# Optimization experiments

Hardware: AMD Instinct MI355X
Metric: run time of the kernel (lower is better)

## Reference

```python
import jax, jax.numpy as jnp
import numpy as np
from jax import lax

# Hardcoded geometry from the module (npatch=4, padding16=1, padding32=2)
GLO_MUL, GLO_RES = 16, 18   # 64/4, 64/4 + 2*1
LOC_MUL, LOC_RES = 32, 36   # 128/4, 128/4 + 2*2
C_FEAT = 16                 # PointNetfeatLocal output channels


def point_to_cell(pts, feat, R):
    """Scatter per-point features into a dense R^3 grid (last write wins,
    matching torch advanced-indexing assignment). pts: (B,N,3) float coords
    already clamped to [0, R-1]; feat: (B,N,C). Returns (B,C,R,R,R)."""
    B, N, C = feat.shape
    idx = pts.astype(jnp.int32)
    bidx = jnp.broadcast_to(jnp.arange(B)[:, None], (B, N))
    grid = jnp.zeros((B, R, R, R, C), feat.dtype)
    grid = grid.at[bidx, idx[..., 0], idx[..., 1], idx[..., 2]].set(feat)
    return jnp.transpose(grid, (0, 4, 1, 2, 3))


def setup_inputs() -> dict:
    key = jax.random.key(0)
    ks = jax.random.split(key, 8)
    B = 4
    # points live in [-0.5, 0.5) so that x*128 + 64.5 lands inside the grid
    curves = jax.random.uniform(ks[0], (B, 8192, 3), jnp.float32) - 0.5
    surfaces = jax.random.uniform(ks[1], (B, 24576, 3), jnp.float32) - 0.5
    occupany64_softmax = jax.random.uniform(ks[2], (B, 2, 64, 64, 64), jnp.float32)
    indices_array = jax.random.randint(ks[3], (B, 16), 0, 64, jnp.int32)
    W1 = jax.random.normal(ks[4], (128, 3), jnp.float32) * 0.1
    b1 = jnp.zeros((128,), jnp.float32)
    W2 = jax.random.normal(ks[5], (16, 128), jnp.float32) * 0.1
    b2 = jnp.zeros((16,), jnp.float32)
    return dict(curves=curves, surfaces=surfaces,
                occupany64_softmax=occupany64_softmax,
                indices_array=indices_array, W1=W1, b1=b1, W2=W2, b2=b2)


def reference(curves, surfaces, occupany64_softmax, indices_array, W1, b1, W2, b2):
    # --- PointNetfeatLocal: two 1x1 Conv1d == per-point MLP 3->128->16 ---
    x = jnp.concatenate([curves, surfaces], axis=1)            # (B, N, 3)
    h = jax.nn.relu(jnp.einsum('bnd,cd->bnc', x, W1) + b1)      # (B, N, 128)
    feat_pt = jnp.einsum('bnc,oc->bno', h, W2) + b2             # (B, N, 16)

    # --- pad occupancy (padding16=1) ---
    occ_pad = jnp.pad(occupany64_softmax,
                      ((0, 0), (0, 0), (1, 1), (1, 1), (1, 1)))  # (B,2,66,66,66)

    # --- batch_grid_pooling128 + padding32=2 ---
    cube128 = jnp.clip(x * 128.0 + 64.5, 0.0, 127.0)
    cell128 = point_to_cell(cube128, feat_pt, 128)              # (B,16,128,128,128)
    cell128_pad = jnp.pad(cell128,
                          ((0, 0), (0, 0), (2, 2), (2, 2), (2, 2)))  # (B,16,132^3)

    # --- crop_global_local_patches (vectorized via vmap'd dynamic_slice) ---
    B, P = indices_array.shape
    bb = jnp.repeat(jnp.arange(B), P)
    pp = indices_array.reshape(-1).astype(jnp.int32)

    def crop_one(b, p):
        i, j, k = p // 16, (p % 16) // 4, p % 4
        g = lax.dynamic_slice(occ_pad,
                              (b, 0, i * GLO_MUL, j * GLO_MUL, k * GLO_MUL),
                              (1, 2, GLO_RES, GLO_RES, GLO_RES))[0]
        l = lax.dynamic_slice(cell128_pad,
                              (b, 0, i * LOC_MUL, j * LOC_MUL, k * LOC_MUL),
                              (1, C_FEAT, LOC_RES, LOC_RES, LOC_RES))[0]
        return g, l

    global_patches, local_patches = jax.vmap(crop_one)(bb, pp)
    # global_patches: (B*P, 2, 18, 18, 18); local_patches: (B*P, 16, 36, 36, 36)
    return global_patches, local_patches
```

## Files before the change

kernel.cpp:

```cpp
#include <hip/hip_runtime.h>

#define BATCH   4
#define NCUR    8192
#define NSUR    24576
#define NPTS    (NCUR + NSUR)
#define NPATCH  64
#define GS      18
#define LS      36
#define GVOL    (GS*GS*GS)
#define LVOL    (LS*LS*LS)
#define GOUT_TOTAL (NPATCH*2*GVOL)
#define GBLOCKS (GOUT_TOTAL/256)
#define MBLOCKS ((BATCH*NPTS)/256)
#define LBLOCKS ((NPATCH*LVOL + 255)/256)

template<int CTRL>
__device__ __forceinline__ float qperm(float x) {
    return __builtin_bit_cast(float, __builtin_amdgcn_mov_dpp(
        __builtin_bit_cast(int, x), CTRL, 0xF, 0xF, true));
}
#define QP_B0 0x00
#define QP_B1 0x55
#define QP_B2 0xAA
#define QP_B3 0xFF
#define QP_X1 0xB1
#define QP_X2 0x4E

__global__ __launch_bounds__(256)
void mlp_scatter_global_kernel(const float* __restrict__ curves,
                               const float* __restrict__ surfaces,
                               const float* __restrict__ W1,
                               const float* __restrict__ b1,
                               const float* __restrict__ W2,
                               const float* __restrict__ b2,
                               const float* __restrict__ occ,
                               const int*   __restrict__ indices,
                               int*   __restrict__ winner,
                               float* __restrict__ feat,
                               float* __restrict__ gout)
{
    int t = threadIdx.x;
    if (blockIdx.x >= MBLOCKS) {
        int gid = (blockIdx.x - MBLOCKS) * 256 + t;
        int z = gid % 18;
        int y = (gid / 18) % 18;
        int x = (gid / 324) % 18;
        int c = (gid / GVOL) & 1;
        int q = gid / (2 * GVOL);

        int b = q >> 4;
        int p = indices[q];
        int i = p >> 4, j = (p >> 2) & 3, k = p & 3;

        int X = i*16 + x - 1;
        int Y = j*16 + y - 1;
        int Z = k*16 + z - 1;
        float v = 0.0f;
        if ((unsigned)X < 64u && (unsigned)Y < 64u && (unsigned)Z < 64u)
            v = occ[((((size_t)b*2 + c)*64 + X)*64 + Y)*64 + Z];
        gout[gid] = v;
        return;
    }

    __shared__ float4 sW1i[128];
    __shared__ float4 sW2i[512];
    __shared__ float4 sb2v[4];
    if (t < 128) {
        int c = t, cc = c & 31, rr = c >> 5;
        sW1i[cc*4 + rr] = make_float4(W1[3*c], W1[3*c+1], W1[3*c+2], b1[c]);
    }
    for (int u = t; u < 2048; u += 256) {
        int o = u >> 7;
        int c = u & 127;
        int cc = c & 31, rr = c >> 5;
        ((float*)sW2i)[(((cc*4 + rr)*4) + (o>>2))*4 + (o&3)] = W2[u];
    }
    if (t < 16) ((float*)sb2v)[t] = b2[t];
    __syncthreads();

    int gid = blockIdx.x * 256 + t;
    int b = gid >> 15;
    int n = gid & (NPTS - 1);

    const float* p;
    if (n < NCUR) p = curves   + ((size_t)b * NCUR + n) * 3;
    else          p = surfaces + ((size_t)b * NSUR + (n - NCUR)) * 3;
    float x0 = p[0], x1 = p[1], x2 = p[2];

    float ax = qperm<QP_B0>(x0), ay = qperm<QP_B0>(x1), az = qperm<QP_B0>(x2);
    float bx = qperm<QP_B1>(x0), by = qperm<QP_B1>(x1), bz = qperm<QP_B1>(x2);
    float gx = qperm<QP_B2>(x0), gy = qperm<QP_B2>(x1), gz = qperm<QP_B2>(x2);
    float dx = qperm<QP_B3>(x0), dy = qperm<QP_B3>(x1), dz = qperm<QP_B3>(x2);

    float acc0[16], acc1[16], acc2[16], acc3[16];
    #pragma unroll
    for (int o = 0; o < 16; ++o) { acc0[o]=0.f; acc1[o]=0.f; acc2[o]=0.f; acc3[o]=0.f; }

    int r = t & 3;
    #pragma unroll 4
    for (int cc = 0; cc < 32; ++cc) {
        int idx = cc*4 + r;
        float4 w1 = sW1i[idx];
        float h0 = fmaxf(fmaf(az, w1.z, fmaf(ay, w1.y, fmaf(ax, w1.x, w1.w))), 0.f);
        float h1 = fmaxf(fmaf(bz, w1.z, fmaf(by, w1.y, fmaf(bx, w1.x, w1.w))), 0.f);
        float h2 = fmaxf(fmaf(gz, w1.z, fmaf(gy, w1.y, fmaf(gx, w1.x, w1.w))), 0.f);
        float h3 = fmaxf(fmaf(dz, w1.z, fmaf(dy, w1.y, fmaf(dx, w1.x, w1.w))), 0.f);
        const float4* w2p = &sW2i[idx*4];
        float4 c0 = w2p[0], c1 = w2p[1], c2 = w2p[2], c3 = w2p[3];
        #define ACC(A, H) \
            A[0]+=H*c0.x;  A[1]+=H*c0.y;  A[2]+=H*c0.z;  A[3]+=H*c0.w;  \
            A[4]+=H*c1.x;  A[5]+=H*c1.y;  A[6]+=H*c1.z;  A[7]+=H*c1.w;  \
            A[8]+=H*c2.x;  A[9]+=H*c2.y;  A[10]+=H*c2.z; A[11]+=H*c2.w; \
            A[12]+=H*c3.x; A[13]+=H*c3.y; A[14]+=H*c3.z; A[15]+=H*c3.w;
        ACC(acc0, h0) ACC(acc1, h1) ACC(acc2, h2) ACC(acc3, h3)
        #undef ACC
    }

    bool r2 = (r & 2) != 0, r1 = (r & 1) != 0;
    float out[16];
    float bb2[16] = { sb2v[0].x, sb2v[0].y, sb2v[0].z, sb2v[0].w,
                      sb2v[1].x, sb2v[1].y, sb2v[1].z, sb2v[1].w,
                      sb2v[2].x, sb2v[2].y, sb2v[2].z, sb2v[2].w,
                      sb2v[3].x, sb2v[3].y, sb2v[3].z, sb2v[3].w };
    #pragma unroll
    for (int o = 0; o < 16; ++o) {
        float sA = r2 ? acc0[o] : acc2[o];
        float sB = r2 ? acc1[o] : acc3[o];
        float C0 = (r2 ? acc2[o] : acc0[o]) + qperm<QP_X2>(sA);
        float C1 = (r2 ? acc3[o] : acc1[o]) + qperm<QP_X2>(sB);
        float v  = r1 ? C0 : C1;
        out[o] = ((r1 ? C1 : C0) + qperm<QP_X1>(v)) + bb2[o];
    }

    float4* fo = (float4*)(feat + (size_t)gid * 16);
    fo[0] = make_float4(out[0],  out[1],  out[2],  out[3]);
    fo[1] = make_float4(out[4],  out[5],  out[6],  out[7]);
    fo[2] = make_float4(out[8],  out[9],  out[10], out[11]);
    fo[3] = make_float4(out[12], out[13], out[14], out[15]);

    float ccx = fminf(fmaxf(__fadd_rn(__fmul_rn(x0, 128.0f), 64.5f), 0.0f), 127.0f);
    float ccy = fminf(fmaxf(__fadd_rn(__fmul_rn(x1, 128.0f), 64.5f), 0.0f), 127.0f);
    float ccz = fminf(fmaxf(__fadd_rn(__fmul_rn(x2, 128.0f), 64.5f), 0.0f), 127.0f);
    int ix = (int)ccx, iy = (int)ccy, iz = (int)ccz;

    atomicMax(winner + ((((size_t)b*128 + ix)*128 + iy)*128 + iz), n);
}

__global__ __launch_bounds__(256)
void local_patch_kernel(const int*   __restrict__ winner,
                        const float* __restrict__ feat,
                        const int*   __restrict__ indices,
                        float* __restrict__ lout)
{
    int gid = blockIdx.x * 256 + threadIdx.x;
    int q = gid / LVOL;
    int s = gid - q * LVOL;
    int z = s % 36;
    int y = (s / 36) % 36;
    int x = s / 1296;

    int b = q >> 4;
    int p = indices[q];
    int i = p >> 4, j = (p >> 2) & 3, k = p & 3;

    int X = i*32 + x - 2;
    int Y = j*32 + y - 2;
    int Z = k*32 + z - 2;

    int w = -1;
    if ((unsigned)X < 128u && (unsigned)Y < 128u && (unsigned)Z < 128u)
        w = winner[(((size_t)b*128 + X)*128 + Y)*128 + Z];

    float vals[16];
    if (w >= 0) {
        const float4* f = (const float4*)(feat + ((size_t)b*NPTS + w)*16);
        float4 a0 = f[0], a1 = f[1], a2 = f[2], a3 = f[3];
        vals[0]=a0.x;  vals[1]=a0.y;  vals[2]=a0.z;  vals[3]=a0.w;
        vals[4]=a1.x;  vals[5]=a1.y;  vals[6]=a1.z;  vals[7]=a1.w;
        vals[8]=a2.x;  vals[9]=a2.y;  vals[10]=a2.z; vals[11]=a2.w;
        vals[12]=a3.x; vals[13]=a3.y; vals[14]=a3.z; vals[15]=a3.w;
    } else {
        #pragma unroll
        for (int c = 0; c < 16; ++c) vals[c] = 0.0f;
    }

    size_t base = (size_t)q * 16 * LVOL + s;
    #pragma unroll
    for (int c = 0; c < 16; ++c)
        lout[base + (size_t)c * LVOL] = vals[c];
}

extern "C" void kernel_launch(void* const* d_in, const int* in_sizes, int n_in,
                              void* d_out, int out_size, void* d_ws, size_t ws_size,
                              hipStream_t stream)
{
    const float* curves   = (const float*)d_in[0];
    const float* surfaces = (const float*)d_in[1];
    const float* occ      = (const float*)d_in[2];
    const int*   indices  = (const int*)  d_in[3];
    const float* W1       = (const float*)d_in[4];
    const float* b1       = (const float*)d_in[5];
    const float* W2       = (const float*)d_in[6];
    const float* b2       = (const float*)d_in[7];

    const size_t winner_bytes = (size_t)BATCH * 128 * 128 * 128 * sizeof(int);
    int*   winner = (int*)d_ws;
    float* feat   = (float*)((char*)d_ws + winner_bytes);


    mlp_scatter_global_kernel<<<MBLOCKS + GBLOCKS, 256, 0, stream>>>(
        curves, surfaces, W1, b1, W2, b2, occ, indices,
        winner, feat, (float*)d_out);

    local_patch_kernel<<<LBLOCKS, 256, 0, stream>>>(
        winner, feat, indices, (float*)d_out + GOUT_TOTAL);
}
```

Baseline: 49.09 us.

## Restructure local patch gather to one block per patch-channel plane with float4 stores

The local patch kernel now assigns one block to each (patch, channel) plane and loops over voxels in groups of four consecutive z positions, writing float4 vectors to the output. Previously each thread handled one voxel and wrote 16 strided scalar stores across channels. The new layout makes output stores wide and contiguous, but it reads the winner grid 16 times (once per channel) and issues scalar strided feature loads, which raises read traffic. Only 1024 blocks are launched, each looping over about 11.6K float4s.

```diff
diff --git a/kernel.cpp b/kernel.cpp
--- a/kernel.cpp
+++ b/kernel.cpp
@@ -12,7 +12,7 @@
 #define GOUT_TOTAL (NPATCH*2*GVOL)
 #define GBLOCKS (GOUT_TOTAL/256)
 #define MBLOCKS ((BATCH*NPTS)/256)
-#define LBLOCKS ((NPATCH*LVOL + 255)/256)
+#define LVOL4   (LVOL/4)
 
 template<int CTRL>
 __device__ __forceinline__ float qperm(float x) {
@@ -147,47 +147,48 @@
 }
 
 __global__ __launch_bounds__(256)
-void local_patch_kernel(const int*   __restrict__ winner,
-                        const float* __restrict__ feat,
-                        const int*   __restrict__ indices,
-                        float* __restrict__ lout)
+void local_patch_plane_kernel(const int*   __restrict__ winner,
+                              const float* __restrict__ feat,
+                              const int*   __restrict__ indices,
+                              float* __restrict__ lout)
 {
-    int gid = blockIdx.x * 256 + threadIdx.x;
-    int q = gid / LVOL;
-    int s = gid - q * LVOL;
-    int z = s % 36;
-    int y = (s / 36) % 36;
-    int x = s / 1296;
+    int q = blockIdx.x >> 4;
+    int c = blockIdx.x & 15;
 
     int b = q >> 4;
     int p = indices[q];
     int i = p >> 4, j = (p >> 2) & 3, k = p & 3;
 
-    int X = i*32 + x - 2;
-    int Y = j*32 + y - 2;
-    int Z = k*32 + z - 2;
-
-    int w = -1;
-    if ((unsigned)X < 128u && (unsigned)Y < 128u && (unsigned)Z < 128u)
-        w = winner[(((size_t)b*128 + X)*128 + Y)*128 + Z];
-
-    float vals[16];
-    if (w >= 0) {
-        const float4* f = (const float4*)(feat + ((size_t)b*NPTS + w)*16);
-        float4 a0 = f[0], a1 = f[1], a2 = f[2], a3 = f[3];
-        vals[0]=a0.x;  vals[1]=a0.y;  vals[2]=a0.z;  vals[3]=a0.w;
-        vals[4]=a1.x;  vals[5]=a1.y;  vals[6]=a1.z;  vals[7]=a1.w;
-        vals[8]=a2.x;  vals[9]=a2.y;  vals[10]=a2.z; vals[11]=a2.w;
-        vals[12]=a3.x; vals[13]=a3.y; vals[14]=a3.z; vals[15]=a3.w;
-    } else {
-        #pragma unroll
-        for (int c = 0; c < 16; ++c) vals[c] = 0.0f;
-    }
-
-    size_t base = (size_t)q * 16 * LVOL + s;
-    #pragma unroll
-    for (int c = 0; c < 16; ++c)
-        lout[base + (size_t)c * LVOL] = vals[c];
+    const int*   wbase = winner + (size_t)b * 128 * 128 * 128;
+    const float* fbase = feat + (size_t)b * NPTS * 16 + c;
+    float4* obase = (float4*)(lout + ((size_t)q * 16 + c) * LVOL);
+
+    for (int v = threadIdx.x; v < LVOL4; v += 256) {
+        int s  = v * 4;
+        int z  = s % 36;
+        int y  = (s / 36) % 36;
+        int x  = s / 1296;
+
+        int X = i*32 + x - 2;
+        int Y = j*32 + y - 2;
+        int Zb = k*32 + z - 2;
+        bool xyok = ((unsigned)X < 128u) & ((unsigned)Y < 128u);
+        const int* wrow = wbase + (((size_t)X*128 + Y) << 7);
+
+        float4 o = make_float4(0.f, 0.f, 0.f, 0.f);
+        if (xyok) {
+            int Z0 = Zb, Z1 = Zb+1, Z2 = Zb+2, Z3 = Zb+3;
+            int w0 = ((unsigned)Z0 < 128u) ? wrow[Z0] : -1;
+            int w1 = ((unsigned)Z1 < 128u) ? wrow[Z1] : -1;
+            int w2 = ((unsigned)Z2 < 128u) ? wrow[Z2] : -1;
+            int w3 = ((unsigned)Z3 < 128u) ? wrow[Z3] : -1;
+            if (w0 >= 0) o.x = fbase[(size_t)w0 * 16];
+            if (w1 >= 0) o.y = fbase[(size_t)w1 * 16];
+            if (w2 >= 0) o.z = fbase[(size_t)w2 * 16];
+            if (w3 >= 0) o.w = fbase[(size_t)w3 * 16];
+        }
+        obase[v] = o;
+    }
 }
 
 extern "C" void kernel_launch(void* const* d_in, const int* in_sizes, int n_in,
@@ -212,6 +213,6 @@
         curves, surfaces, W1, b1, W2, b2, occ, indices,
         winner, feat, (float*)d_out);
 
-    local_patch_kernel<<<LBLOCKS, 256, 0, stream>>>(
+    local_patch_plane_kernel<<<NPATCH * 16, 256, 0, stream>>>(
         winner, feat, indices, (float*)d_out + GOUT_TOTAL);
 }
```

New measurement: 73.87 us. +50.5%, slower.
